# Kernel tuning notes

Hardware: AMD Instinct MI355X
Metric: run time of the kernel (lower is better)

Reference implementation:

```python
import jax, jax.numpy as jnp
import numpy as np

BETA = 1.0

def setup_inputs() -> dict:
    key = jax.random.key(0)
    k1, k2, k3 = jax.random.split(key, 3)
    B, T, G, D, V = 4, 2048, 8, 128, 1024
    inputs = jax.random.normal(k1, (B, T, G * D), dtype=jnp.float32)
    paddings = jax.random.randint(k2, (B, T), 0, 2, dtype=jnp.int32)
    codebook = jax.random.normal(k3, (V, G, D), dtype=jnp.float32)  # (V, G, D)
    return {"inputs": inputs, "paddings": paddings, "codebook": codebook}

def reference(inputs, paddings, codebook):
    B, T, _ = inputs.shape
    V, G, D = codebook.shape
    sg = jax.lax.stop_gradient
    x = inputs.reshape(B, T, G, D)
    x2 = jnp.sum(x * x, axis=-1)                      # (B,T,G)
    c2 = jnp.sum(codebook * codebook, axis=-1)        # (V,G)
    xc = jnp.einsum('btgd,vgd->btvg', x, codebook)    # (B,T,V,G) GEMM
    dist = x2[:, :, None, :] - 2.0 * xc + c2[None, None]
    ids = jnp.argmin(dist, axis=2)                    # (B,T,G) int
    # gather codebook[ids[b,t,g], g] -> (B,T,G,D)
    quantized = codebook[ids, jnp.arange(G)[None, None, :]]
    mask = (1 - paddings).astype(jnp.float32)[:, :, None, None]  # (B,T,1,1)
    msum = mask.sum()
    kmeans_loss = jnp.sum(((quantized - sg(x)) ** 2) * mask) / msum
    commitment_loss = jnp.sum(((x - sg(quantized)) ** 2) * mask) / msum
    total_loss = kmeans_loss + BETA * commitment_loss
    quantized_st = ((x + sg(quantized - x)) * mask).reshape(B, T, G * D)
    ids = jnp.where((paddings == 1)[:, :, None], -1, ids.astype(jnp.int32))
    return (ids, quantized_st, kmeans_loss, commitment_loss, total_loss)
```

## Files before the change

### kernel.cpp

```cpp
#include <hip/hip_runtime.h>
#include <math.h>

typedef _Float16 f16;
typedef f16 half8 __attribute__((ext_vector_type(8)));
typedef float f32x4 __attribute__((ext_vector_type(4)));

#define BT 8192
#define NG 8
#define ND 128
#define NV 1024
#define MARGIN  0.08f
#define MARGIN3 0.16f
#define BM 64
#define BN 64
#define NT 16
#define FULLBIT 0x40000000u

#define OUT_IDS 0
#define OUT_Q   65536
#define OUT_L   (65536 + 8388608)

#define OFF_C2A    0
#define OFF_C2B    8192
#define OFF_LOSSG  81920
#define OFF_CNT    147456
#define OFF_FLAGS  147464
#define OFF_CBH    213000
#define OFF_PART   (OFF_CBH + 524288)
#define OFF_CAND2  (OFF_PART + 64)
#define OFF_TOKMAP (OFF_CAND2 + 65536)

__device__ __forceinline__ void gll16(const f16* g, f16* l) {
    __builtin_amdgcn_global_load_lds(
        (const __attribute__((address_space(1))) unsigned int*)g,
        (__attribute__((address_space(3))) unsigned int*)l, 16, 0, 0);
}

__global__ __launch_bounds__(256) void prep_kernel(
    const float* __restrict__ cb, const int* __restrict__ pad,
    f16* __restrict__ cbh, float* __restrict__ c2a, float* __restrict__ c2b,
    int* __restrict__ cnt, int* __restrict__ tokmap,
    float* __restrict__ out_ids, float* __restrict__ out_q,
    float* __restrict__ lossg) {
    const int tid = threadIdx.x;

    if (blockIdx.x == 512) {
        __shared__ int ps[256];
        const int base = tid * 32;
        int c = 0;
#pragma unroll
        for (int i = 0; i < 32; ++i) c += 1 - pad[base + i];
        ps[tid] = c;
        __syncthreads();
        for (int st = 1; st < 256; st <<= 1) {
            int v = (tid >= st) ? ps[tid - st] : 0;
            __syncthreads();
            ps[tid] += v;
            __syncthreads();
        }
        int o = ps[tid] - c;
        if (tid == 255) {
            cnt[1] = ps[255];
            cnt[0] = 0;
        }
        for (int i = 0; i < 32; ++i) {
            int tok = base + i;
            if (!pad[tok]) tokmap[o++] = tok;
        }
        return;
    }

    if (blockIdx.x > 512) {
        const int gt = (blockIdx.x - 513) * 256 + tid;
        const float4 z = make_float4(0.f, 0.f, 0.f, 0.f);
#pragma unroll 4
        for (int i = gt; i < BT * NG * ND / 4; i += 512 * 256) {
            int tok = i >> 8;
            if (pad[tok]) ((float4*)out_q)[i] = z;
        }
        if (gt < BT * NG) {
            int tok = gt >> 3;
            if (pad[tok]) {
                out_ids[gt] = -1.0f;
                lossg[gt] = 0.0f;
            }
        }
        return;
    }

    __shared__ float prod[16][16][9];
    __shared__ float rbuf[16][8];
    const int rloc = tid >> 4, t = tid & 15;
    const int idx = blockIdx.x * 16 + rloc;
    const int v = idx >> 3, g = idx & 7;
    const int rl = v & 63;
    const float4* row4 = (const float4*)(cb + (size_t)idx * ND);

    float4 a = row4[t * 2], b = row4[t * 2 + 1];
    float vv[8] = {a.x, a.y, a.z, a.w, b.x, b.y, b.z, b.w};
    half8 h;
#pragma unroll
    for (int e = 0; e < 8; ++e) {
        prod[rloc][t][e] = __fmul_rn(vv[e], vv[e]);
        h[e] = (f16)vv[e];
    }
    int cn = v >> 6;
    size_t base = ((size_t)(g * 16 + cn)) * 8192 + rl * 128;
    *(half8*)(cbh + base + ((t ^ (rl & 7)) * 8)) = h;
    __syncthreads();

    if (t < 8) {
        float r = 0.f;
#pragma unroll
        for (int tt = 0; tt < 16; ++tt)
            r = __fadd_rn(r, prod[rloc][tt][t]);
        rbuf[rloc][t] = r;
    }
    __syncthreads();
    if (t == 0) {
        float s = __fadd_rn(
            __fadd_rn(__fadd_rn(rbuf[rloc][0], rbuf[rloc][1]),
                      __fadd_rn(rbuf[rloc][2], rbuf[rloc][3])),
            __fadd_rn(__fadd_rn(rbuf[rloc][4], rbuf[rloc][5]),
                      __fadd_rn(rbuf[rloc][6], rbuf[rloc][7])));
        c2a[idx] = s;
        c2b[g * NV + v] = s;
    }
}

__global__ __launch_bounds__(256, 2) void mfma_gemm(
    const float* __restrict__ x, const f16* __restrict__ cbh,
    const float* __restrict__ cb, const float* __restrict__ c2b,
    const int* __restrict__ ncnt, const int* __restrict__ tokmap,
    float* __restrict__ out_ids, float* __restrict__ out_q,
    float* __restrict__ lossg, int* __restrict__ cnt,
    int* __restrict__ flags, int* __restrict__ cand2) {
    __shared__ __align__(16) f16 Bh[3][BN * ND];
    __shared__ __align__(16) float c2s[NV];
    __shared__ int idsL[BM];
    __shared__ int tokL[BM];

    const int tid = threadIdx.x;
    const int b = blockIdx.x;
    const int g = b & 7;
    const int count = *ncnt;
    const int tile_base = (b >> 3) * BM;
    if (tile_base >= count) return;
    const int lane = tid & 63;
    const int w = tid >> 6;
    const int wr = w & 1, wc = w >> 1;
    const int l15 = lane & 15, l4 = lane >> 4;

    ((float4*)c2s)[tid] = ((const float4*)(c2b + (size_t)g * NV))[tid];
    {
        const f16* sh0 = cbh + ((size_t)(g * 16 + 0)) * 8192;
#pragma unroll
        for (int it = 0; it < 4; ++it)
            gll16(sh0 + it * 2048 + tid * 8, &Bh[0][it * 2048 + tid * 8]);
        const f16* sh1 = cbh + ((size_t)(g * 16 + 1)) * 8192;
#pragma unroll
        for (int it = 0; it < 4; ++it)
            gll16(sh1 + it * 2048 + tid * 8, &Bh[1][it * 2048 + tid * 8]);
    }

    int tokA_[2];
#pragma unroll
    for (int ti = 0; ti < 2; ++ti) {
        int slot = tile_base + wr * 32 + ti * 16 + l15;
        tokA_[ti] = tokmap[(slot < count) ? slot : 0];
    }

    half8 ah[4][2];
#pragma unroll
    for (int kk = 0; kk < 4; ++kk)
#pragma unroll
        for (int ti = 0; ti < 2; ++ti) {
            const float* ap = x + ((size_t)tokA_[ti] * NG + g) * ND
                              + kk * 32 + l4 * 8;
            float4 p0 = *(const float4*)ap, p1 = *(const float4*)(ap + 4);
            float vv[8] = {p0.x, p0.y, p0.z, p0.w, p1.x, p1.y, p1.z, p1.w};
            half8 h;
#pragma unroll
            for (int j = 0; j < 8; ++j) h[j] = (f16)vv[j];
            ah[kk][ti] = h;
        }

    float d1s[2][4], d2s[2][4], d3s[2][4];
    int id1s[2][4], id2s[2][4];
#pragma unroll
    for (int ti = 0; ti < 2; ++ti)
#pragma unroll
        for (int r = 0; r < 4; ++r) {
            d1s[ti][r] = INFINITY;
            d2s[ti][r] = INFINITY;
            d3s[ti][r] = INFINITY;
            id1s[ti][r] = 0;
            id2s[ti][r] = 0;
        }

    int buf = 0;
#pragma unroll 1
    for (int t = 0; t < NT; ++t) {
        if (t < NT - 1)
            asm volatile("s_waitcnt vmcnt(8) lgkmcnt(0)" ::: "memory");
        else
            asm volatile("s_waitcnt vmcnt(0) lgkmcnt(0)" ::: "memory");
        __builtin_amdgcn_s_barrier();
        __builtin_amdgcn_sched_barrier(0);

        if (t + 2 < NT) {
            int nb = buf + 2;
            nb = (nb >= 3) ? nb - 3 : nb;
            const f16* sh = cbh + ((size_t)(g * 16 + t + 2)) * 8192;
#pragma unroll
            for (int it = 0; it < 4; ++it)
                gll16(sh + it * 2048 + tid * 8,
                      &Bh[nb][it * 2048 + tid * 8]);
        }

        f32x4 acc[2][2];
#pragma unroll
        for (int ti = 0; ti < 2; ++ti)
#pragma unroll
            for (int tj = 0; tj < 2; ++tj)
                acc[ti][tj] = (f32x4){0.f, 0.f, 0.f, 0.f};

#pragma unroll
        for (int kk = 0; kk < 4; ++kk) {
            half8 bh[2];
#pragma unroll
            for (int tj = 0; tj < 2; ++tj) {
                int rw = wc * 32 + tj * 16 + l15;
                bh[tj] = *(const half8*)(
                    &Bh[buf][rw * 128 + (((kk * 4 + l4) ^ (rw & 7)) << 3)]);
            }
#pragma unroll
            for (int ti = 0; ti < 2; ++ti)
#pragma unroll
                for (int tj = 0; tj < 2; ++tj)
                    acc[ti][tj] = __builtin_amdgcn_mfma_f32_16x16x32_f16(
                        ah[kk][ti], bh[tj], acc[ti][tj], 0, 0, 0);
        }

#pragma unroll
        for (int tj = 0; tj < 2; ++tj) {
            int code = t * BN + wc * 32 + tj * 16 + l15;
            float c2v = c2s[code];
#pragma unroll
            for (int ti = 0; ti < 2; ++ti)
#pragma unroll
                for (int r = 0; r < 4; ++r) {
                    float dv = fmaf(-2.0f, acc[ti][tj][r], c2v);
                    bool lt1 = dv < d1s[ti][r];
                    bool lt2 = dv < d2s[ti][r];
                    bool lt3 = dv < d3s[ti][r];
                    d3s[ti][r] = lt2 ? d2s[ti][r] : (lt3 ? dv : d3s[ti][r]);
                    d2s[ti][r] = lt1 ? d1s[ti][r] : (lt2 ? dv : d2s[ti][r]);
                    id2s[ti][r] = lt1 ? id1s[ti][r] : (lt2 ? code : id2s[ti][r]);
                    d1s[ti][r] = lt1 ? dv : d1s[ti][r];
                    id1s[ti][r] = lt1 ? code : id1s[ti][r];
                }
        }
        buf = (buf == 2) ? 0 : buf + 1;
    }

    __syncthreads();
    float4* red = (float4*)&Bh[0][0];
    float* redd3 = (float*)(red + 128);
#pragma unroll
    for (int ti = 0; ti < 2; ++ti)
#pragma unroll
        for (int r = 0; r < 4; ++r) {
            float d1 = d1s[ti][r], d2 = d2s[ti][r], d3 = d3s[ti][r];
            int i1 = id1s[ti][r], i2 = id2s[ti][r];
#pragma unroll
            for (int m = 1; m < 16; m <<= 1) {
                float od1 = __shfl_xor(d1, m);
                float od2 = __shfl_xor(d2, m);
                float od3 = __shfl_xor(d3, m);
                int oi1 = __shfl_xor(i1, m);
                int oi2 = __shfl_xor(i2, m);
                bool ow = od1 < d1;
                float w1 = ow ? od1 : d1, w2 = ow ? od2 : d2, w3 = ow ? od3 : d3;
                int wi1 = ow ? oi1 : i1, wi2 = ow ? oi2 : i2;
                float l1 = ow ? d1 : od1, l2 = ow ? d2 : od2;
                int li1 = ow ? i1 : oi1;
                d1 = w1; i1 = wi1;
                bool t2 = w2 < l1;
                d2 = t2 ? w2 : l1;
                i2 = t2 ? wi2 : li1;
                d3 = t2 ? fminf(w3, l1) : fminf(w2, l2);
            }
            if (l15 == 0) {
                int o = wc * BM + wr * 32 + ti * 16 + l4 * 4 + r;
                red[o] = make_float4(d1, __int_as_float(i1), d2,
                                     __int_as_float(i2));
                redd3[o] = d3;
            }
        }
    __syncthreads();

    if (tid < BM) {
        float4 A = red[tid], C = red[BM + tid];
        float a3 = redd3[tid], c3 = redd3[BM + tid];
        float a1 = A.x, a2 = A.z, c1 = C.x, c2q = C.z;
        int ai1 = __float_as_int(A.y), ai2 = __float_as_int(A.w);
        int ci1 = __float_as_int(C.y), ci2 = __float_as_int(C.w);
        bool cw = c1 < a1;
        float w1 = cw ? c1 : a1, w2 = cw ? c2q : a2, w3 = cw ? c3 : a3;
        int wi1 = cw ? ci1 : ai1, wi2 = cw ? ci2 : ai2;
        float l1 = cw ? a1 : c1, l2 = cw ? a2 : c2q;
        int li1 = cw ? ai1 : ci1;
        float d1 = w1;
        int i1 = wi1;
        bool t2 = w2 < l1;
        float d2 = t2 ? w2 : l1;
        int i2 = t2 ? wi2 : li1;
        float d3 = t2 ? fminf(w3, l1) : fminf(w2, l2);

        int slot = tile_base + tid;
        if (slot < count) {
            int tok = tokmap[slot];
            int idx = tok * NG + g;
            out_ids[idx] = (float)i1;
            idsL[tid] = i1;
            tokL[tid] = tok;
            if (d2 - d1 < MARGIN) {
                int pos = atomicAdd(cnt, 1);
                flags[pos] = idx;
                cand2[idx] = i2 | ((d3 - d1 < MARGIN3) ? (int)FULLBIT : 0);
            }
        } else {
            idsL[tid] = -1;
        }
    }
    __syncthreads();

#pragma unroll
    for (int it = 0; it < 8; ++it) {
        int i = it * 256 + tid;
        int tl = i >> 5, d4 = i & 31;
        int id = idsL[tl];
        if (id >= 0) {
            int tok = tokL[tl];
            size_t rowo = ((size_t)tok * NG + g) * ND;
            float4 q = ((const float4*)(cb + ((size_t)id * NG + g) * ND))[d4];
            float4 a = ((const float4*)(x + rowo))[d4];
            float e0 = q.x - a.x, e1 = q.y - a.y;
            float e2 = q.z - a.z, e3 = q.w - a.w;
            float s = e0 * e0 + e1 * e1 + e2 * e2 + e3 * e3;
            ((float4*)(out_q + rowo))[d4] = q;
#pragma unroll
            for (int m = 1; m < 32; m <<= 1) s += __shfl_xor(s, m);
            if (d4 == 0) lossg[tok * NG + g] = s;
        }
    }
}

__global__ __launch_bounds__(256) void recheck(
    const float* __restrict__ x, const float* __restrict__ cb,
    const float* __restrict__ c2w, const int* __restrict__ cnt,
    const int* __restrict__ flags, const int* __restrict__ cand2,
    float* __restrict__ out_ids, float* __restrict__ out_q,
    float* __restrict__ lossg) {
    __shared__ __align__(16) float xs[ND];
    __shared__ float2 redw[4];
    __shared__ int bidS;
    const int tid = threadIdx.x;
    const int lane = tid & 63;
    const int w = tid >> 6;
    const int n_f = cnt[0];

    for (int f = blockIdx.x * 4 + w; f < n_f; f += gridDim.x * 4) {
        int idx = flags[f];
        unsigned cc = (unsigned)cand2[idx];
        if (cc & FULLBIT) continue;
        int g = idx & 7;
        int id1 = (int)out_ids[idx];
        int id2 = (int)(cc & ~FULLBIT);
        float2 xv = ((const float2*)(x + (size_t)idx * ND))[lane];
        float2 av = ((const float2*)(cb + ((size_t)id1 * NG + g) * ND))[lane];
        float2 bv = ((const float2*)(cb + ((size_t)id2 * NG + g) * ND))[lane];
        float eA0 = xv.x - av.x, eA1 = xv.y - av.y;
        float eB0 = xv.x - bv.x, eB1 = xv.y - bv.y;
        float sA = eA0 * eA0 + eA1 * eA1;
        float sB = eB0 * eB0 + eB1 * eB1;
#pragma unroll
        for (int m = 1; m < 64; m <<= 1) {
            sA += __shfl_xor(sA, m);
            sB += __shfl_xor(sB, m);
        }
        int win;
        float sw;
        if (sA < sB) { win = id1; sw = sA; }
        else if (sB < sA) { win = id2; sw = sB; }
        else { win = (id1 < id2) ? id1 : id2; sw = sA; }
        if (win != id1) {
            if (lane == 0) {
                out_ids[idx] = (float)win;
                lossg[idx] = sw;
            }
            if (lane < 32) {
                float4 q = ((const float4*)(cb + ((size_t)win * NG + g) * ND))[lane];
                ((float4*)(out_q + (size_t)idx * ND))[lane] = q;
            }
        }
    }
    __syncthreads();

    for (int f = blockIdx.x; f < n_f; f += gridDim.x) {
        int idx = flags[f];
        if (!(((unsigned)cand2[idx]) & FULLBIT)) continue;
        int g = idx & 7;
        __syncthreads();
        if (tid < 32)
            ((float4*)xs)[tid] = ((const float4*)(x + (size_t)idx * ND))[tid];
        __syncthreads();

        float rr[8];
#pragma unroll
        for (int j = 0; j < 8; ++j) rr[j] = 0.0f;
#pragma unroll
        for (int i = 0; i < 32; ++i) {
            float4 v = ((const float4*)xs)[i];
            int j0 = (i * 4) & 7;
            rr[j0 + 0] = __fadd_rn(rr[j0 + 0], __fmul_rn(v.x, v.x));
            rr[j0 + 1] = __fadd_rn(rr[j0 + 1], __fmul_rn(v.y, v.y));
            rr[j0 + 2] = __fadd_rn(rr[j0 + 2], __fmul_rn(v.z, v.z));
            rr[j0 + 3] = __fadd_rn(rr[j0 + 3], __fmul_rn(v.w, v.w));
        }
        float x2v = __fadd_rn(
            __fadd_rn(__fadd_rn(rr[0], rr[1]), __fadd_rn(rr[2], rr[3])),
            __fadd_rn(__fadd_rn(rr[4], rr[5]), __fadd_rn(rr[6], rr[7])));

        float best = INFINITY;
        int bid = 0x7FFFFFFF;
        float s0 = 0.f, s1 = 0.f, s2 = 0.f, s3 = 0.f;
#pragma unroll
        for (int i = 0; i < 32; ++i) {
            float4 a = ((const float4*)xs)[i];
            float4 q0 = ((const float4*)(cb + ((size_t)(tid) * NG + g) * ND))[i];
            float4 q1 = ((const float4*)(cb + ((size_t)(tid + 256) * NG + g) * ND))[i];
            float4 q2 = ((const float4*)(cb + ((size_t)(tid + 512) * NG + g) * ND))[i];
            float4 q3 = ((const float4*)(cb + ((size_t)(tid + 768) * NG + g) * ND))[i];
            s0 = fmaf(a.x, q0.x, s0); s0 = fmaf(a.y, q0.y, s0);
            s0 = fmaf(a.z, q0.z, s0); s0 = fmaf(a.w, q0.w, s0);
            s1 = fmaf(a.x, q1.x, s1); s1 = fmaf(a.y, q1.y, s1);
            s1 = fmaf(a.z, q1.z, s1); s1 = fmaf(a.w, q1.w, s1);
            s2 = fmaf(a.x, q2.x, s2); s2 = fmaf(a.y, q2.y, s2);
            s2 = fmaf(a.z, q2.z, s2); s2 = fmaf(a.w, q2.w, s2);
            s3 = fmaf(a.x, q3.x, s3); s3 = fmaf(a.y, q3.y, s3);
            s3 = fmaf(a.z, q3.z, s3); s3 = fmaf(a.w, q3.w, s3);
        }
        float dd[4] = {s0, s1, s2, s3};
#pragma unroll
        for (int jj = 0; jj < 4; ++jj) {
            int c = tid + 256 * jj;
            float d = __fadd_rn(__fsub_rn(x2v, __fmul_rn(2.0f, dd[jj])),
                                c2w[(size_t)c * NG + g]);
            if (d < best || (d == best && c < bid)) { best = d; bid = c; }
        }
#pragma unroll
        for (int m = 1; m < 64; m <<= 1) {
            float od = __shfl_xor(best, m);
            int ob = __shfl_xor(bid, m);
            if (od < best || (od == best && ob < bid)) { best = od; bid = ob; }
        }
        if (lane == 0) redw[w] = make_float2(best, __int_as_float(bid));
        __syncthreads();
        if (tid == 0) {
            float b2 = redw[0].x;
            int i2 = __float_as_int(redw[0].y);
#pragma unroll
            for (int ww = 1; ww < 4; ++ww) {
                float ob = redw[ww].x;
                int oi = __float_as_int(redw[ww].y);
                if (ob < b2 || (ob == b2 && oi < i2)) { b2 = ob; i2 = oi; }
            }
            out_ids[idx] = (float)i2;
            bidS = i2;
        }
        __syncthreads();
        if (tid < 32) {
            float4 q = ((const float4*)(cb + ((size_t)bidS * NG + g) * ND))[tid];
            ((float4*)(out_q + (size_t)idx * ND))[tid] = q;
            float4 a = ((const float4*)xs)[tid];
            float e0 = q.x - a.x, e1 = q.y - a.y;
            float e2 = q.z - a.z, e3 = q.w - a.w;
            float s = e0 * e0 + e1 * e1 + e2 * e2 + e3 * e3;
#pragma unroll
            for (int m = 1; m < 32; m <<= 1) s += __shfl_xor(s, m);
            if (tid == 0) lossg[idx] = s;
        }
    }
}

__global__ __launch_bounds__(256) void loss_part(
    const float* __restrict__ lossg, float* __restrict__ part) {
    __shared__ float sr[256];
    const int tid = threadIdx.x;
    float4 v = ((const float4*)lossg)[blockIdx.x * 256 + tid];
    sr[tid] = ((v.x + v.y) + (v.z + v.w));
    __syncthreads();
    for (int st = 128; st > 0; st >>= 1) {
        if (tid < st) sr[tid] += sr[tid + st];
        __syncthreads();
    }
    if (tid == 0) part[blockIdx.x] = sr[0];
}

__global__ __launch_bounds__(64) void final_kernel(
    const int* __restrict__ cnt, const float* __restrict__ part,
    float* __restrict__ out_l) {
    const int tid = threadIdx.x;
    float s = part[tid];
#pragma unroll
    for (int m = 1; m < 64; m <<= 1) s += __shfl_xor(s, m);
    if (tid == 0) {
        float k = s / (float)cnt[1];
        out_l[0] = k;
        out_l[1] = k;
        out_l[2] = k + k;
    }
}

extern "C" void kernel_launch(void* const* d_in, const int* in_sizes, int n_in,
                              void* d_out, int out_size, void* d_ws, size_t ws_size,
                              hipStream_t stream) {
    const float* x = (const float*)d_in[0];
    const int* pad = (const int*)d_in[1];
    const float* cb = (const float*)d_in[2];
    float* out = (float*)d_out;
    float* ws = (float*)d_ws;

    float* ws_c2a = ws + OFF_C2A;
    float* ws_c2b = ws + OFF_C2B;
    float* ws_lossg = ws + OFF_LOSSG;
    int* ws_cnt = (int*)(ws + OFF_CNT);
    int* ws_flags = (int*)(ws + OFF_FLAGS);
    f16* cbh = (f16*)(ws + OFF_CBH);
    float* ws_part = ws + OFF_PART;
    int* ws_cand2 = (int*)(ws + OFF_CAND2);
    int* ws_tokmap = (int*)(ws + OFF_TOKMAP);

    prep_kernel<<<1025, 256, 0, stream>>>(cb, pad, cbh, ws_c2a, ws_c2b,
                                          ws_cnt, ws_tokmap, out + OUT_IDS,
                                          out + OUT_Q, ws_lossg);
    mfma_gemm<<<(BT / BM) * NG, 256, 0, stream>>>(x, cbh, cb, ws_c2b,
                                                  ws_cnt + 1, ws_tokmap,
                                                  out + OUT_IDS, out + OUT_Q,
                                                  ws_lossg, ws_cnt, ws_flags,
                                                  ws_cand2);
    recheck<<<512, 256, 0, stream>>>(x, cb, ws_c2a, ws_cnt, ws_flags,
                                     ws_cand2, out + OUT_IDS, out + OUT_Q,
                                     ws_lossg);
    loss_part<<<64, 256, 0, stream>>>(ws_lossg, ws_part);
    final_kernel<<<1, 64, 0, stream>>>(ws_cnt, ws_part, out + OUT_L);
}
```

Baseline: 73.49 us.

## Double GEMM block to 512 threads, splitting codebook columns across eight waves

The nearest-code GEMM block grows from 4 to 8 waves. Each wave now covers 16 codebook columns instead of 32, so its accumulators and B-fragment loads are halved. The per-tile async loads, the wait counts, the cross-wave top-2/top-3 reduction (now over 4 column groups) and the epilogue loop are adjusted to match. The aim is more waves to hide latency and fewer registers per wave, at the cost of duplicated A-fragment loads and a larger reduction.

```diff
diff --git a/kernel.cpp b/kernel.cpp
--- a/kernel.cpp
+++ b/kernel.cpp
@@ -128,7 +128,7 @@
     }
 }
 
-__global__ __launch_bounds__(256, 2) void mfma_gemm(
+__global__ __launch_bounds__(512, 4) void mfma_gemm(
     const float* __restrict__ x, const f16* __restrict__ cbh,
     const float* __restrict__ cb, const float* __restrict__ c2b,
     const int* __restrict__ ncnt, const int* __restrict__ tokmap,
@@ -148,19 +148,19 @@
     if (tile_base >= count) return;
     const int lane = tid & 63;
     const int w = tid >> 6;
-    const int wr = w & 1, wc = w >> 1;
+    const int wr = w & 1;
+    const int wc = w >> 1;
     const int l15 = lane & 15, l4 = lane >> 4;
-
-    ((float4*)c2s)[tid] = ((const float4*)(c2b + (size_t)g * NV))[tid];
+    const int rw = wc * 16 + l15;
+
+    ((float2*)c2s)[tid] = ((const float2*)(c2b + (size_t)g * NV))[tid];
     {
         const f16* sh0 = cbh + ((size_t)(g * 16 + 0)) * 8192;
-#pragma unroll
-        for (int it = 0; it < 4; ++it)
-            gll16(sh0 + it * 2048 + tid * 8, &Bh[0][it * 2048 + tid * 8]);
+        gll16(sh0 + tid * 8, &Bh[0][tid * 8]);
+        gll16(sh0 + 4096 + tid * 8, &Bh[0][4096 + tid * 8]);
         const f16* sh1 = cbh + ((size_t)(g * 16 + 1)) * 8192;
-#pragma unroll
-        for (int it = 0; it < 4; ++it)
-            gll16(sh1 + it * 2048 + tid * 8, &Bh[1][it * 2048 + tid * 8]);
+        gll16(sh1 + tid * 8, &Bh[1][tid * 8]);
+        gll16(sh1 + 4096 + tid * 8, &Bh[1][4096 + tid * 8]);
     }
 
     int tokA_[2];
@@ -202,7 +202,7 @@
 #pragma unroll 1
     for (int t = 0; t < NT; ++t) {
         if (t < NT - 1)
-            asm volatile("s_waitcnt vmcnt(8) lgkmcnt(0)" ::: "memory");
+            asm volatile("s_waitcnt vmcnt(2) lgkmcnt(0)" ::: "memory");
         else
             asm volatile("s_waitcnt vmcnt(0) lgkmcnt(0)" ::: "memory");
         __builtin_amdgcn_s_barrier();
@@ -212,45 +212,32 @@
             int nb = buf + 2;
             nb = (nb >= 3) ? nb - 3 : nb;
             const f16* sh = cbh + ((size_t)(g * 16 + t + 2)) * 8192;
-#pragma unroll
-            for (int it = 0; it < 4; ++it)
-                gll16(sh + it * 2048 + tid * 8,
-                      &Bh[nb][it * 2048 + tid * 8]);
-        }
-
-        f32x4 acc[2][2];
-#pragma unroll
-        for (int ti = 0; ti < 2; ++ti)
-#pragma unroll
-            for (int tj = 0; tj < 2; ++tj)
-                acc[ti][tj] = (f32x4){0.f, 0.f, 0.f, 0.f};
+            gll16(sh + tid * 8, &Bh[nb][tid * 8]);
+            gll16(sh + 4096 + tid * 8, &Bh[nb][4096 + tid * 8]);
+        }
+
+        f32x4 acc[2];
+#pragma unroll
+        for (int ti = 0; ti < 2; ++ti) acc[ti] = (f32x4){0.f, 0.f, 0.f, 0.f};
 
 #pragma unroll
         for (int kk = 0; kk < 4; ++kk) {
-            half8 bh[2];
-#pragma unroll
-            for (int tj = 0; tj < 2; ++tj) {
-                int rw = wc * 32 + tj * 16 + l15;
-                bh[tj] = *(const half8*)(
-                    &Bh[buf][rw * 128 + (((kk * 4 + l4) ^ (rw & 7)) << 3)]);
-            }
+            half8 bh = *(const half8*)(
+                &Bh[buf][rw * 128 + (((kk * 4 + l4) ^ (rw & 7)) << 3)]);
 #pragma unroll
             for (int ti = 0; ti < 2; ++ti)
-#pragma unroll
-                for (int tj = 0; tj < 2; ++tj)
-                    acc[ti][tj] = __builtin_amdgcn_mfma_f32_16x16x32_f16(
-                        ah[kk][ti], bh[tj], acc[ti][tj], 0, 0, 0);
-        }
-
-#pragma unroll
-        for (int tj = 0; tj < 2; ++tj) {
-            int code = t * BN + wc * 32 + tj * 16 + l15;
+                acc[ti] = __builtin_amdgcn_mfma_f32_16x16x32_f16(
+                    ah[kk][ti], bh, acc[ti], 0, 0, 0);
+        }
+
+        {
+            int code = t * BN + rw;
             float c2v = c2s[code];
 #pragma unroll
             for (int ti = 0; ti < 2; ++ti)
 #pragma unroll
                 for (int r = 0; r < 4; ++r) {
-                    float dv = fmaf(-2.0f, acc[ti][tj][r], c2v);
+                    float dv = fmaf(-2.0f, acc[ti][r], c2v);
                     bool lt1 = dv < d1s[ti][r];
                     bool lt2 = dv < d2s[ti][r];
                     bool lt3 = dv < d3s[ti][r];
@@ -266,7 +253,7 @@
 
     __syncthreads();
     float4* red = (float4*)&Bh[0][0];
-    float* redd3 = (float*)(red + 128);
+    float* redd3 = (float*)(red + 256);
 #pragma unroll
     for (int ti = 0; ti < 2; ++ti)
 #pragma unroll
@@ -301,22 +288,25 @@
     __syncthreads();
 
     if (tid < BM) {
-        float4 A = red[tid], C = red[BM + tid];
-        float a3 = redd3[tid], c3 = redd3[BM + tid];
-        float a1 = A.x, a2 = A.z, c1 = C.x, c2q = C.z;
-        int ai1 = __float_as_int(A.y), ai2 = __float_as_int(A.w);
-        int ci1 = __float_as_int(C.y), ci2 = __float_as_int(C.w);
-        bool cw = c1 < a1;
-        float w1 = cw ? c1 : a1, w2 = cw ? c2q : a2, w3 = cw ? c3 : a3;
-        int wi1 = cw ? ci1 : ai1, wi2 = cw ? ci2 : ai2;
-        float l1 = cw ? a1 : c1, l2 = cw ? a2 : c2q;
-        int li1 = cw ? ai1 : ci1;
-        float d1 = w1;
-        int i1 = wi1;
-        bool t2 = w2 < l1;
-        float d2 = t2 ? w2 : l1;
-        int i2 = t2 ? wi2 : li1;
-        float d3 = t2 ? fminf(w3, l1) : fminf(w2, l2);
+        float4 A = red[tid];
+        float d1 = A.x, d2 = A.z, d3 = redd3[tid];
+        int i1 = __float_as_int(A.y), i2 = __float_as_int(A.w);
+#pragma unroll
+        for (int ww = 1; ww < 4; ++ww) {
+            float4 C = red[ww * BM + tid];
+            float e1 = C.x, e2 = C.z, e3 = redd3[ww * BM + tid];
+            int j1 = __float_as_int(C.y), j2 = __float_as_int(C.w);
+            bool ow = e1 < d1;
+            float w1 = ow ? e1 : d1, w2 = ow ? e2 : d2, w3 = ow ? e3 : d3;
+            int wi1 = ow ? j1 : i1, wi2 = ow ? j2 : i2;
+            float l1 = ow ? d1 : e1, l2 = ow ? d2 : e2;
+            int li1 = ow ? i1 : j1;
+            d1 = w1; i1 = wi1;
+            bool t2 = w2 < l1;
+            d2 = t2 ? w2 : l1;
+            i2 = t2 ? wi2 : li1;
+            d3 = t2 ? fminf(w3, l1) : fminf(w2, l2);
+        }
 
         int slot = tile_base + tid;
         if (slot < count) {
@@ -337,8 +327,8 @@
     __syncthreads();
 
 #pragma unroll
-    for (int it = 0; it < 8; ++it) {
-        int i = it * 256 + tid;
+    for (int it = 0; it < 4; ++it) {
+        int i = it * 512 + tid;
         int tl = i >> 5, d4 = i & 31;
         int id = idsL[tl];
         if (id >= 0) {
@@ -546,7 +536,7 @@
     prep_kernel<<<1025, 256, 0, stream>>>(cb, pad, cbh, ws_c2a, ws_c2b,
                                           ws_cnt, ws_tokmap, out + OUT_IDS,
                                           out + OUT_Q, ws_lossg);
-    mfma_gemm<<<(BT / BM) * NG, 256, 0, stream>>>(x, cbh, cb, ws_c2b,
+    mfma_gemm<<<(BT / BM) * NG, 512, 0, stream>>>(x, cbh, cb, ws_c2b,
                                                   ws_cnt + 1, ws_tokmap,
                                                   out + OUT_IDS, out + OUT_Q,
                                                   ws_lossg, ws_cnt, ws_flags,
```

After: 76.88 us. 1.05x slower.
